# Kernel optimization log

Measured on AMD Instinct MI355X. Metric: run time of the kernel, lower is better.

Reference implementation:

```python
import jax, jax.numpy as jnp
import numpy as np

B, T, N, K, d = 8, 12, 325, 8, 64
D = K * d


def setup_inputs() -> dict:
    key = jax.random.key(0)
    ks = jax.random.split(key, 12)
    s = 0.02
    f32 = jnp.float32
    inp = {
        "X": jax.random.normal(ks[0], (B, T, N, D), f32),
        "STE": jax.random.normal(ks[1], (B, T, N, D), f32),
        "Wq": (jax.random.normal(ks[2], (2 * D, D), f32) * s),
        "bq": jnp.zeros((D,), f32),
        "Wk": (jax.random.normal(ks[3], (2 * D, D), f32) * s),
        "bk": jnp.zeros((D,), f32),
        "Wv": (jax.random.normal(ks[4], (2 * D, D), f32) * s),
        "bv": jnp.zeros((D,), f32),
        "W1": (jax.random.normal(ks[5], (D, D), f32) * s),
        "b1": jnp.zeros((D,), f32),
        "W2": (jax.random.normal(ks[6], (D, D), f32) * s),
        "b2": jnp.zeros((D,), f32),
        "attn_mask": 0,
    }
    return inp


def reference(X, STE, Wq, bq, Wk, bk, Wv, bv, W1, b1, W2, b2, attn_mask):
    # X, STE: [B, T, N, D]
    Xc = jnp.concatenate([X, STE], axis=-1)          # [B,T,N,2D]
    q = jax.nn.relu(Xc @ Wq + bq).reshape(B, T, N, K, d)
    k = jax.nn.relu(Xc @ Wk + bk).reshape(B, T, N, K, d)
    v = jax.nn.relu(Xc @ Wv + bv).reshape(B, T, N, K, d)

    # scores: [B, K, T, N, N] (attention over spatial/node axis N)
    scores = jnp.einsum('btnhe,btmhe->bhtnm', q, k)
    # mask_flag=False -> TriangularCausalMask applied (upper-tri masked with -inf)
    causal = jnp.triu(jnp.ones((N, N), dtype=bool), 1)
    scores = jnp.where(causal, -jnp.inf, scores)
    # original scales AFTER masking; -inf / sqrt(d) stays -inf
    scores = scores / jnp.sqrt(jnp.asarray(d, scores.dtype))
    attn = jax.nn.softmax(scores, axis=-1)
    # dropout: eval mode (identity)

    ctx = jnp.einsum('bhtnm,btmhe->btnhe', attn, v).reshape(B, T, N, D)
    out = jax.nn.relu(ctx @ W1 + b1) @ W2 + b2        # [B,T,N,D]

    # match torch's head-major cat(dim=0): [K*B, T, N, N]
    attn_full = jnp.transpose(attn, (1, 0, 2, 3, 4)).reshape(K * B, T, N, N)
    return out, attn_full
```

## Files before the change

### kernel.cpp

```cpp
#include <hip/hip_runtime.h>
#include <hip/hip_bf16.h>

typedef __hip_bfloat16 bf16;
using f32x4  = __attribute__((ext_vector_type(4))) float;
using short8 = __attribute__((ext_vector_type(8))) short;

#define M_ROWS   31200
#define M_PAD    31232
#define N_TOK    325
#define D_MODEL  512
#define QKV_LD   1536

#define GLOBAL_AS(p) ((const __attribute__((address_space(1))) unsigned int*)(p))
#define LDS_AS(p)    ((__attribute__((address_space(3))) unsigned int*)(p))

__global__ void init_flag(int* flag) { if (threadIdx.x == 0) *flag = 0; }

__global__ void detect_dtype(const unsigned short* __restrict__ x, int* flag)
{
    int i = blockIdx.x * 256 + threadIdx.x;
    unsigned short h = x[i];
    int e = (h >> 7) & 0xFF;
    if (e >= 135) atomicOr(flag, 1);
}

__device__ __forceinline__ float load_in(const void* p, size_t i, bool f32)
{
    return f32 ? ((const float*)p)[i] : __bfloat162float(((const bf16*)p)[i]);
}

__global__ void concat_cast(const void* __restrict__ X, const void* __restrict__ STE,
                            bf16* __restrict__ Xc, const int* __restrict__ flag)
{
    const bool f32 = (*flag != 0);
    int idx = blockIdx.x * 256 + threadIdx.x;
    int r = idx >> 7, c8 = (idx & 127) << 3;
    short8 v = {0, 0, 0, 0, 0, 0, 0, 0};
    if (r < M_ROWS) {
        const void* src = (c8 < 512) ? X : STE;
        int cc = c8 & 511;
        if (f32) {
            const float* s = (const float*)src + (size_t)r * 512 + cc;
            float4 a = *(const float4*)s;
            float4 b = *(const float4*)(s + 4);
            ((bf16*)&v)[0] = __float2bfloat16(a.x); ((bf16*)&v)[1] = __float2bfloat16(a.y);
            ((bf16*)&v)[2] = __float2bfloat16(a.z); ((bf16*)&v)[3] = __float2bfloat16(a.w);
            ((bf16*)&v)[4] = __float2bfloat16(b.x); ((bf16*)&v)[5] = __float2bfloat16(b.y);
            ((bf16*)&v)[6] = __float2bfloat16(b.z); ((bf16*)&v)[7] = __float2bfloat16(b.w);
        } else {
            v = *(const short8*)((const bf16*)src + (size_t)r * 512 + cc);
        }
    }
    *(short8*)&Xc[(size_t)r * 1024 + c8] = v;
}

__global__ void transpose_w_tiled(const void* __restrict__ src, bf16* __restrict__ dst,
                                  int krows, int ncols, const int* __restrict__ flag)
{
    __shared__ float tile[32][33];
    const bool f32 = (*flag != 0);
    const int kt = blockIdx.y * 32, nt = blockIdx.x * 32;
    const int tx = threadIdx.x & 31, ty = threadIdx.x >> 5;
#pragma unroll
    for (int r = 0; r < 32; r += 8)
        tile[ty + r][tx] = load_in(src, (size_t)(kt + ty + r) * ncols + (nt + tx), f32);
    __syncthreads();
#pragma unroll
    for (int r = 0; r < 32; r += 8)
        dst[(size_t)(nt + ty + r) * krows + (kt + tx)] = __float2bfloat16(tile[tx][ty + r]);
}

__global__ void prep_bias(const void* __restrict__ bq, const void* __restrict__ bk,
                          const void* __restrict__ bv, const void* __restrict__ b1,
                          const void* __restrict__ b2,
                          float* __restrict__ biasQKV, float* __restrict__ b1f,
                          float* __restrict__ b2f, const int* __restrict__ flag)
{
    const bool f32 = (*flag != 0);
    int i = blockIdx.x * 256 + threadIdx.x;
    if (i < 512) {
        biasQKV[i]        = load_in(bq, i, f32);
        biasQKV[512 + i]  = load_in(bk, i, f32);
        biasQKV[1024 + i] = load_in(bv, i, f32);
        b1f[i] = load_in(b1, i, f32);
        b2f[i] = load_in(b2, i, f32);
    }
}

template<int OUTF32>
__global__ __launch_bounds__(256) void gemm_lds(
    const bf16* __restrict__ A, int lda,
    const bf16* __restrict__ Bt, int ldb,
    const float* __restrict__ bias, void* __restrict__ Cv,
    int Mvalid, int Kdim, int ldc, int do_relu, int nby)
{
    __shared__ alignas(16) bf16 As0[128 * 32];
    __shared__ alignas(16) bf16 As1[128 * 32];
    __shared__ alignas(16) bf16 Bs0[128 * 32];
    __shared__ alignas(16) bf16 Bs1[128 * 32];
    const int cpx = gridDim.x >> 3;
    const int swz = (blockIdx.x & 7) * cpx + (blockIdx.x >> 3);
    const int m0 = (swz / nby) * 128;
    const int n0 = (swz % nby) * 128;
    const int t = threadIdx.x, wave = t >> 6, lane = t & 63;
    const int wm = (wave >> 1) * 64, wn = (wave & 1) * 64;
    const int lrow = lane & 15, lk8 = (lane >> 4) * 8;
    const int srow = lane >> 2, scol = (lane & 3) << 3;
    f32x4 acc[4][4] = {};
    const int nk = Kdim >> 6;

    for (int ks = 0; ks < nk; ++ks) {
        const int kk = ks << 6;
        __syncthreads();
#pragma unroll
        for (int c = 0; c < 2; ++c) {
            const int chunk = wave * 2 + c;
            const bf16* ga = A  + (size_t)(m0 + chunk * 16 + srow) * lda + kk + scol;
            const bf16* gb = Bt + (size_t)(n0 + chunk * 16 + srow) * ldb + kk + scol;
            __builtin_amdgcn_global_load_lds(GLOBAL_AS(ga),      LDS_AS(As0 + chunk * 512), 16, 0, 0);
            __builtin_amdgcn_global_load_lds(GLOBAL_AS(ga + 32), LDS_AS(As1 + chunk * 512), 16, 0, 0);
            __builtin_amdgcn_global_load_lds(GLOBAL_AS(gb),      LDS_AS(Bs0 + chunk * 512), 16, 0, 0);
            __builtin_amdgcn_global_load_lds(GLOBAL_AS(gb + 32), LDS_AS(Bs1 + chunk * 512), 16, 0, 0);
        }
        __syncthreads();
        short8 af[4], bfr[4];
#pragma unroll
        for (int i = 0; i < 4; ++i) {
            af[i]  = *(const short8*)&As0[(wm + i * 16 + lrow) * 32 + lk8];
            bfr[i] = *(const short8*)&Bs0[(wn + i * 16 + lrow) * 32 + lk8];
        }
#pragma unroll
        for (int i = 0; i < 4; ++i)
#pragma unroll
            for (int j = 0; j < 4; ++j)
                acc[i][j] = __builtin_amdgcn_mfma_f32_16x16x32_bf16(
                    af[i], bfr[j], acc[i][j], 0, 0, 0);
#pragma unroll
        for (int i = 0; i < 4; ++i) {
            af[i]  = *(const short8*)&As1[(wm + i * 16 + lrow) * 32 + lk8];
            bfr[i] = *(const short8*)&Bs1[(wn + i * 16 + lrow) * 32 + lk8];
        }
#pragma unroll
        for (int i = 0; i < 4; ++i)
#pragma unroll
            for (int j = 0; j < 4; ++j)
                acc[i][j] = __builtin_amdgcn_mfma_f32_16x16x32_bf16(
                    af[i], bfr[j], acc[i][j], 0, 0, 0);
    }

    const int r4 = (lane >> 4) * 4;
#pragma unroll
    for (int i = 0; i < 4; ++i) {
#pragma unroll
        for (int r = 0; r < 4; ++r) {
            int grow = m0 + wm + i * 16 + r4 + r;
            if (OUTF32 && grow >= Mvalid) continue;
#pragma unroll
            for (int j = 0; j < 4; ++j) {
                int gcol = n0 + wn + j * 16 + lrow;
                float v  = acc[i][j][r] + bias[gcol];
                if (do_relu) v = fmaxf(v, 0.0f);
                if (OUTF32)
                    ((float*)Cv)[(size_t)grow * ldc + gcol] = v;
                else
                    ((bf16*)Cv)[(size_t)grow * ldc + gcol] = __float2bfloat16(v);
            }
        }
    }
}

__global__ __launch_bounds__(512) void gemm_lds256(
    const bf16* __restrict__ A, int lda,
    const bf16* __restrict__ Bt, int ldb,
    const float* __restrict__ bias, bf16* __restrict__ C,
    int Kdim, int ldc, int nby)
{
    __shared__ alignas(16) bf16 As0[256 * 32];
    __shared__ alignas(16) bf16 As1[256 * 32];
    __shared__ alignas(16) bf16 Bs0[128 * 32];
    __shared__ alignas(16) bf16 Bs1[128 * 32];
    const int cpx = gridDim.x >> 3;
    const int swz = (blockIdx.x & 7) * cpx + (blockIdx.x >> 3);
    const int m0 = (swz / nby) * 256;
    const int n0 = (swz % nby) * 128;
    const int t = threadIdx.x, wave = t >> 6, lane = t & 63;
    const int wm = (wave >> 1) * 64, wn = (wave & 1) * 64;
    const int lrow = lane & 15, lk8 = (lane >> 4) * 8;
    const int srow = lane >> 2, scol = (lane & 3) << 3;
    f32x4 acc[4][4] = {};
    const int nk = Kdim >> 6;

    for (int ks = 0; ks < nk; ++ks) {
        const int kk = ks << 6;
        __syncthreads();
#pragma unroll
        for (int c = 0; c < 2; ++c) {
            const int arow = wave * 32 + c * 16;
            const bf16* ga = A + (size_t)(m0 + arow + srow) * lda + kk + scol;
            __builtin_amdgcn_global_load_lds(GLOBAL_AS(ga),      LDS_AS(As0 + arow * 32), 16, 0, 0);
            __builtin_amdgcn_global_load_lds(GLOBAL_AS(ga + 32), LDS_AS(As1 + arow * 32), 16, 0, 0);
        }
        {
            const int brow = wave * 16;
            const bf16* gb = Bt + (size_t)(n0 + brow + srow) * ldb + kk + scol;
            __builtin_amdgcn_global_load_lds(GLOBAL_AS(gb),      LDS_AS(Bs0 + brow * 32), 16, 0, 0);
            __builtin_amdgcn_global_load_lds(GLOBAL_AS(gb + 32), LDS_AS(Bs1 + brow * 32), 16, 0, 0);
        }
        __syncthreads();
        short8 af[4], bfr[4];
#pragma unroll
        for (int i = 0; i < 4; ++i) {
            af[i]  = *(const short8*)&As0[(wm + i * 16 + lrow) * 32 + lk8];
            bfr[i] = *(const short8*)&Bs0[(wn + i * 16 + lrow) * 32 + lk8];
        }
#pragma unroll
        for (int i = 0; i < 4; ++i)
#pragma unroll
            for (int j = 0; j < 4; ++j)
                acc[i][j] = __builtin_amdgcn_mfma_f32_16x16x32_bf16(
                    af[i], bfr[j], acc[i][j], 0, 0, 0);
#pragma unroll
        for (int i = 0; i < 4; ++i) {
            af[i]  = *(const short8*)&As1[(wm + i * 16 + lrow) * 32 + lk8];
            bfr[i] = *(const short8*)&Bs1[(wn + i * 16 + lrow) * 32 + lk8];
        }
#pragma unroll
        for (int i = 0; i < 4; ++i)
#pragma unroll
            for (int j = 0; j < 4; ++j)
                acc[i][j] = __builtin_amdgcn_mfma_f32_16x16x32_bf16(
                    af[i], bfr[j], acc[i][j], 0, 0, 0);
    }

    const int r4 = (lane >> 4) * 4;
#pragma unroll
    for (int i = 0; i < 4; ++i) {
#pragma unroll
        for (int r = 0; r < 4; ++r) {
            int grow = m0 + wm + i * 16 + r4 + r;
#pragma unroll
            for (int j = 0; j < 4; ++j) {
                int gcol = n0 + wn + j * 16 + lrow;
                float v  = fmaxf(acc[i][j][r] + bias[gcol], 0.0f);
                C[(size_t)grow * ldc + gcol] = __float2bfloat16(v);
            }
        }
    }
}

#define KS_LD  72
#define VT_LD  354
__global__ __launch_bounds__(512) void attn_kernel(
    bf16* __restrict__ qkv, float* __restrict__ attn_out)
{
    __shared__ alignas(16) bf16 Ks[336 * KS_LD];
    __shared__ alignas(16) bf16 Vt[64 * VT_LD + 32];
    __shared__ alignas(16) bf16 ptile[8][16 * 40];
    const int t = threadIdx.x, lane = t & 63, w = t >> 6;
    const int h = blockIdx.x & 7, bt = blockIdx.x >> 3;
    const size_t rowbase = (size_t)bt * N_TOK;
    const int lrow = lane & 15, lk8 = (lane >> 4) * 8;
    const int r4 = (lane >> 4) * 4;
    const int b = bt / 12, tt2 = bt % 12;
    const size_t hb_base = (((size_t)(h * 8 + b)) * 12 + tt2) * N_TOK;

    for (int task = t; task < 336 * 8; task += 512) {
        int m = task >> 3, e0 = (task & 7) << 3;
        short8 v = {0, 0, 0, 0, 0, 0, 0, 0};
        if (m < N_TOK)
            v = *(const short8*)(qkv + (rowbase + m) * QKV_LD + 512 + h * 64 + e0);
        *(short8*)&Ks[m * KS_LD + e0] = v;
    }
    for (int task = t; task < 352 * 8; task += 512) {
        int m = task >> 3, e0 = (task & 7) << 3;
        short8 v = {0, 0, 0, 0, 0, 0, 0, 0};
        if (m < N_TOK)
            v = *(const short8*)(qkv + (rowbase + m) * QKV_LD + 1024 + h * 64 + e0);
#pragma unroll
        for (int j = 0; j < 8; ++j)
            Vt[(e0 + j) * VT_LD + m] = ((bf16*)&v)[j];
    }
    __syncthreads();

    for (int it = 0; it < 3; ++it) {
        if (it == 2 && w > 4) break;
        const int tile = (it < 2) ? (w + it * 8) : (20 - w);
        const int r0 = tile * 16;

        int qrow = r0 + lrow; if (qrow > N_TOK - 1) qrow = N_TOK - 1;
        const bf16* qp = qkv + (rowbase + qrow) * QKV_LD + h * 64 + lk8;
        short8 qa0 = *(const short8*)(qp);
        short8 qa1 = *(const short8*)(qp + 32);

        f32x4 f[22];
        f[21] = (f32x4){0.f, 0.f, 0.f, 0.f};
#pragma unroll
        for (int ct = 0; ct < 21; ++ct) {
            if (ct <= tile) {
                f32x4 a = {0.f, 0.f, 0.f, 0.f};
                short8 kb0 = *(const short8*)&Ks[(ct * 16 + lrow) * KS_LD + lk8];
                short8 kb1 = *(const short8*)&Ks[(ct * 16 + lrow) * KS_LD + 32 + lk8];
                a = __builtin_amdgcn_mfma_f32_16x16x32_bf16(qa0, kb0, a, 0, 0, 0);
                a = __builtin_amdgcn_mfma_f32_16x16x32_bf16(qa1, kb1, a, 0, 0, 0);
                f[ct] = a;
            }
        }

        float mx[4] = {-1e30f, -1e30f, -1e30f, -1e30f};
        float sm[4] = {0.f, 0.f, 0.f, 0.f};
#pragma unroll
        for (int ct = 0; ct < 21; ++ct) {
            if (ct <= tile) {
                const int c = ct * 16 + lrow;
#pragma unroll
                for (int r = 0; r < 4; ++r)
                    if (c <= r0 + r4 + r) mx[r] = fmaxf(mx[r], f[ct][r]);
            }
        }
#pragma unroll
        for (int r = 0; r < 4; ++r) {
#pragma unroll
            for (int o = 1; o < 16; o <<= 1) mx[r] = fmaxf(mx[r], __shfl_xor(mx[r], o));
        }
#pragma unroll
        for (int ct = 0; ct < 21; ++ct) {
            if (ct <= tile) {
                const int c = ct * 16 + lrow;
#pragma unroll
                for (int r = 0; r < 4; ++r) {
                    float e = (c <= r0 + r4 + r)
                                  ? __expf((f[ct][r] - mx[r]) * 0.125f) : 0.f;
                    f[ct][r] = e;
                    sm[r] += e;
                }
            }
        }
#pragma unroll
        for (int r = 0; r < 4; ++r) {
#pragma unroll
            for (int o = 1; o < 16; o <<= 1) sm[r] += __shfl_xor(sm[r], o);
            sm[r] = 1.0f / sm[r];
        }
#pragma unroll
        for (int ct = 0; ct < 21; ++ct) {
            if (ct <= tile) {
#pragma unroll
                for (int r = 0; r < 4; ++r) f[ct][r] *= sm[r];
            }
        }

#pragma unroll
        for (int ct = 0; ct < 21; ++ct) {
            const int c = ct * 16 + lrow;
            if (c < N_TOK) {
#pragma unroll
                for (int r = 0; r < 4; ++r) {
                    const int n = r0 + r4 + r;
                    if (n < N_TOK) {
                        float v = (ct <= tile && c <= n) ? f[ct][r] : 0.f;
                        attn_out[(hb_base + n) * N_TOK + c] = v;
                    }
                }
            }
        }

        f32x4 acc[4] = {};
        bf16* pt = &ptile[w][0];
#pragma unroll
        for (int s = 0; s < 11; ++s) {
            if (s <= (tile >> 1)) {
#pragma unroll
                for (int half = 0; half < 2; ++half) {
                    const int ct2 = 2 * s + half;
                    const int c = ct2 * 16 + lrow;
#pragma unroll
                    for (int r = 0; r < 4; ++r) {
                        const int n = r0 + r4 + r;
                        float v = (ct2 <= tile && c <= n) ? f[ct2][r] : 0.f;
                        pt[(r4 + r) * 40 + half * 16 + lrow] = __float2bfloat16(v);
                    }
                }
                short8 aa = *(const short8*)&pt[lrow * 40 + lk8];
#pragma unroll
                for (int e = 0; e < 4; ++e) {
                    short8 bb = *(const short8*)&Vt[(e * 16 + lrow) * VT_LD + s * 32 + lk8];
                    acc[e] = __builtin_amdgcn_mfma_f32_16x16x32_bf16(aa, bb, acc[e], 0, 0, 0);
                }
            }
        }

#pragma unroll
        for (int e = 0; e < 4; ++e) {
#pragma unroll
            for (int r = 0; r < 4; ++r) {
                const int n = r0 + r4 + r;
                if (n < N_TOK)
                    qkv[(rowbase + n) * QKV_LD + h * 64 + e * 16 + lrow] =
                        __float2bfloat16(acc[e][r]);
            }
        }
    }
}

extern "C" void kernel_launch(void* const* d_in, const int* in_sizes, int n_in,
                              void* d_out, int out_size, void* d_ws, size_t ws_size,
                              hipStream_t stream)
{
    const void* X   = d_in[0];
    const void* STE = d_in[1];
    const void* Wq  = d_in[2];
    const void* bq  = d_in[3];
    const void* Wk  = d_in[4];
    const void* bk  = d_in[5];
    const void* Wv  = d_in[6];
    const void* bv  = d_in[7];
    const void* W1  = d_in[8];
    const void* b1  = d_in[9];
    const void* W2  = d_in[10];
    const void* b2  = d_in[11];

    float* out0     = (float*)d_out;
    float* attn_out = (float*)d_out + (size_t)M_ROWS * D_MODEL;
    bf16*  Xc       = (bf16*)attn_out;

    char* ws = (char*)d_ws;
    bf16*  qkv   = (bf16*)(ws);
    bf16*  BtQKV = (bf16*)(ws + 95944704);
    bf16*  W1T   = (bf16*)(ws + 99090432);
    bf16*  W2T   = (bf16*)(ws + 99614720);
    float* biasQ = (float*)(ws + 100139008);
    float* b1f   = (float*)(ws + 100145152);
    float* b2f   = (float*)(ws + 100147200);
    int*   flag  = (int*)(ws + 100149248);
    bf16*  hbuf  = qkv + 512;

    init_flag<<<1, 64, 0, stream>>>(flag);
    detect_dtype<<<64, 256, 0, stream>>>((const unsigned short*)X, flag);

    transpose_w_tiled<<<dim3(16, 32), 256, 0, stream>>>(Wq, BtQKV, 1024, 512, flag);
    transpose_w_tiled<<<dim3(16, 32), 256, 0, stream>>>(Wk, BtQKV + 512 * 1024, 1024, 512, flag);
    transpose_w_tiled<<<dim3(16, 32), 256, 0, stream>>>(Wv, BtQKV + 1024 * 1024, 1024, 512, flag);
    transpose_w_tiled<<<dim3(16, 16), 256, 0, stream>>>(W1, W1T, 512, 512, flag);
    transpose_w_tiled<<<dim3(16, 16), 256, 0, stream>>>(W2, W2T, 512, 512, flag);
    prep_bias<<<2, 256, 0, stream>>>(bq, bk, bv, b1, b2, biasQ, b1f, b2f, flag);

    concat_cast<<<(M_PAD * 128) / 256, 256, 0, stream>>>(X, STE, Xc, flag);

    gemm_lds256<<<122 * 12, 512, 0, stream>>>(
        Xc, 1024, BtQKV, 1024, biasQ, qkv, 1024, QKV_LD, 12);

    attn_kernel<<<768, 512, 0, stream>>>(qkv, attn_out);

    gemm_lds<0><<<244 * 4, 256, 0, stream>>>(
        qkv, QKV_LD, W1T, 512, b1f, hbuf, M_PAD, 512, QKV_LD, 1, 4);

    gemm_lds<1><<<244 * 4, 256, 0, stream>>>(
        hbuf, QKV_LD, W2T, 512, b2f, out0, M_ROWS, 512, D_MODEL, 0, 4);
}
```

Measured before the change: 403.4 us.

## Fuse concat/cast into QKV GEMM and use 256-row tiles for FFN GEMMs

Removes the separate concat_cast kernel. The QKV GEMM now reads X and STE directly, converts fp32 to bf16 in registers and stores the A tiles to LDS, which avoids writing and re-reading a 64MB bf16 intermediate. The two FFN GEMMs move from the 128x128 kernel to the templated 256x128 kernel with 512 threads, halving the block count. The trade-off is that the A loads are now synchronous register loads instead of async global_load_lds, which may expose latency inside the GEMM main loop.

```diff
diff --git a/kernel.cpp b/kernel.cpp
--- a/kernel.cpp
+++ b/kernel.cpp
@@ -27,31 +27,6 @@
 __device__ __forceinline__ float load_in(const void* p, size_t i, bool f32)
 {
     return f32 ? ((const float*)p)[i] : __bfloat162float(((const bf16*)p)[i]);
-}
-
-__global__ void concat_cast(const void* __restrict__ X, const void* __restrict__ STE,
-                            bf16* __restrict__ Xc, const int* __restrict__ flag)
-{
-    const bool f32 = (*flag != 0);
-    int idx = blockIdx.x * 256 + threadIdx.x;
-    int r = idx >> 7, c8 = (idx & 127) << 3;
-    short8 v = {0, 0, 0, 0, 0, 0, 0, 0};
-    if (r < M_ROWS) {
-        const void* src = (c8 < 512) ? X : STE;
-        int cc = c8 & 511;
-        if (f32) {
-            const float* s = (const float*)src + (size_t)r * 512 + cc;
-            float4 a = *(const float4*)s;
-            float4 b = *(const float4*)(s + 4);
-            ((bf16*)&v)[0] = __float2bfloat16(a.x); ((bf16*)&v)[1] = __float2bfloat16(a.y);
-            ((bf16*)&v)[2] = __float2bfloat16(a.z); ((bf16*)&v)[3] = __float2bfloat16(a.w);
-            ((bf16*)&v)[4] = __float2bfloat16(b.x); ((bf16*)&v)[5] = __float2bfloat16(b.y);
-            ((bf16*)&v)[6] = __float2bfloat16(b.z); ((bf16*)&v)[7] = __float2bfloat16(b.w);
-        } else {
-            v = *(const short8*)((const bf16*)src + (size_t)r * 512 + cc);
-        }
-    }
-    *(short8*)&Xc[(size_t)r * 1024 + c8] = v;
 }
 
 __global__ void transpose_w_tiled(const void* __restrict__ src, bf16* __restrict__ dst,
@@ -87,40 +62,65 @@
     }
 }
 
-template<int OUTF32>
-__global__ __launch_bounds__(256) void gemm_lds(
-    const bf16* __restrict__ A, int lda,
-    const bf16* __restrict__ Bt, int ldb,
-    const float* __restrict__ bias, void* __restrict__ Cv,
-    int Mvalid, int Kdim, int ldc, int do_relu, int nby)
-{
-    __shared__ alignas(16) bf16 As0[128 * 32];
-    __shared__ alignas(16) bf16 As1[128 * 32];
+__global__ __launch_bounds__(512) void gemm_qkv(
+    const void* __restrict__ Xv, const void* __restrict__ STEv,
+    const bf16* __restrict__ Bt, const float* __restrict__ bias,
+    bf16* __restrict__ C, const int* __restrict__ flag)
+{
+    __shared__ alignas(16) bf16 As0[256 * 32];
+    __shared__ alignas(16) bf16 As1[256 * 32];
     __shared__ alignas(16) bf16 Bs0[128 * 32];
     __shared__ alignas(16) bf16 Bs1[128 * 32];
+    const bool f32 = (*flag != 0);
     const int cpx = gridDim.x >> 3;
     const int swz = (blockIdx.x & 7) * cpx + (blockIdx.x >> 3);
-    const int m0 = (swz / nby) * 128;
-    const int n0 = (swz % nby) * 128;
+    const int m0 = (swz / 12) * 256;
+    const int n0 = (swz % 12) * 128;
     const int t = threadIdx.x, wave = t >> 6, lane = t & 63;
     const int wm = (wave >> 1) * 64, wn = (wave & 1) * 64;
     const int lrow = lane & 15, lk8 = (lane >> 4) * 8;
     const int srow = lane >> 2, scol = (lane & 3) << 3;
     f32x4 acc[4][4] = {};
-    const int nk = Kdim >> 6;
-
-    for (int ks = 0; ks < nk; ++ks) {
+
+    for (int ks = 0; ks < 16; ++ks) {
         const int kk = ks << 6;
+        const void* src = (kk < 512) ? Xv : STEv;
+        const int kc = kk & 511;
         __syncthreads();
 #pragma unroll
         for (int c = 0; c < 2; ++c) {
-            const int chunk = wave * 2 + c;
-            const bf16* ga = A  + (size_t)(m0 + chunk * 16 + srow) * lda + kk + scol;
-            const bf16* gb = Bt + (size_t)(n0 + chunk * 16 + srow) * ldb + kk + scol;
-            __builtin_amdgcn_global_load_lds(GLOBAL_AS(ga),      LDS_AS(As0 + chunk * 512), 16, 0, 0);
-            __builtin_amdgcn_global_load_lds(GLOBAL_AS(ga + 32), LDS_AS(As1 + chunk * 512), 16, 0, 0);
-            __builtin_amdgcn_global_load_lds(GLOBAL_AS(gb),      LDS_AS(Bs0 + chunk * 512), 16, 0, 0);
-            __builtin_amdgcn_global_load_lds(GLOBAL_AS(gb + 32), LDS_AS(Bs1 + chunk * 512), 16, 0, 0);
+            const int arow = wave * 32 + c * 16;
+            const int grow = m0 + arow + srow;
+            short8 va0 = {0,0,0,0,0,0,0,0}, va1 = {0,0,0,0,0,0,0,0};
+            if (grow < M_ROWS) {
+                if (f32) {
+                    const float* s = (const float*)src + (size_t)grow * 512 + kc + scol;
+                    float4 a0 = *(const float4*)(s);
+                    float4 a1 = *(const float4*)(s + 4);
+                    float4 b0 = *(const float4*)(s + 32);
+                    float4 b1 = *(const float4*)(s + 36);
+                    ((bf16*)&va0)[0] = __float2bfloat16(a0.x); ((bf16*)&va0)[1] = __float2bfloat16(a0.y);
+                    ((bf16*)&va0)[2] = __float2bfloat16(a0.z); ((bf16*)&va0)[3] = __float2bfloat16(a0.w);
+                    ((bf16*)&va0)[4] = __float2bfloat16(a1.x); ((bf16*)&va0)[5] = __float2bfloat16(a1.y);
+                    ((bf16*)&va0)[6] = __float2bfloat16(a1.z); ((bf16*)&va0)[7] = __float2bfloat16(a1.w);
+                    ((bf16*)&va1)[0] = __float2bfloat16(b0.x); ((bf16*)&va1)[1] = __float2bfloat16(b0.y);
+                    ((bf16*)&va1)[2] = __float2bfloat16(b0.z); ((bf16*)&va1)[3] = __float2bfloat16(b0.w);
+                    ((bf16*)&va1)[4] = __float2bfloat16(b1.x); ((bf16*)&va1)[5] = __float2bfloat16(b1.y);
+                    ((bf16*)&va1)[6] = __float2bfloat16(b1.z); ((bf16*)&va1)[7] = __float2bfloat16(b1.w);
+                } else {
+                    const bf16* s = (const bf16*)src + (size_t)grow * 512 + kc + scol;
+                    va0 = *(const short8*)(s);
+                    va1 = *(const short8*)(s + 32);
+                }
+            }
+            *(short8*)&As0[(arow + srow) * 32 + scol] = va0;
+            *(short8*)&As1[(arow + srow) * 32 + scol] = va1;
+        }
+        {
+            const int brow = wave * 16;
+            const bf16* gb = Bt + (size_t)(n0 + brow + srow) * 1024 + kk + scol;
+            __builtin_amdgcn_global_load_lds(GLOBAL_AS(gb),      LDS_AS(Bs0 + brow * 32), 16, 0, 0);
+            __builtin_amdgcn_global_load_lds(GLOBAL_AS(gb + 32), LDS_AS(Bs1 + brow * 32), 16, 0, 0);
         }
         __syncthreads();
         short8 af[4], bfr[4];
@@ -154,26 +154,22 @@
 #pragma unroll
         for (int r = 0; r < 4; ++r) {
             int grow = m0 + wm + i * 16 + r4 + r;
-            if (OUTF32 && grow >= Mvalid) continue;
 #pragma unroll
             for (int j = 0; j < 4; ++j) {
                 int gcol = n0 + wn + j * 16 + lrow;
-                float v  = acc[i][j][r] + bias[gcol];
-                if (do_relu) v = fmaxf(v, 0.0f);
-                if (OUTF32)
-                    ((float*)Cv)[(size_t)grow * ldc + gcol] = v;
-                else
-                    ((bf16*)Cv)[(size_t)grow * ldc + gcol] = __float2bfloat16(v);
-            }
-        }
-    }
-}
-
+                float v  = fmaxf(acc[i][j][r] + bias[gcol], 0.0f);
+                C[(size_t)grow * QKV_LD + gcol] = __float2bfloat16(v);
+            }
+        }
+    }
+}
+
+template<int OUTF32, int RELU>
 __global__ __launch_bounds__(512) void gemm_lds256(
     const bf16* __restrict__ A, int lda,
     const bf16* __restrict__ Bt, int ldb,
-    const float* __restrict__ bias, bf16* __restrict__ C,
-    int Kdim, int ldc, int nby)
+    const float* __restrict__ bias, void* __restrict__ Cv,
+    int Mvalid, int Kdim, int ldc, int nby)
 {
     __shared__ alignas(16) bf16 As0[256 * 32];
     __shared__ alignas(16) bf16 As1[256 * 32];
@@ -238,11 +234,16 @@
 #pragma unroll
         for (int r = 0; r < 4; ++r) {
             int grow = m0 + wm + i * 16 + r4 + r;
+            if (OUTF32 && grow >= Mvalid) continue;
 #pragma unroll
             for (int j = 0; j < 4; ++j) {
                 int gcol = n0 + wn + j * 16 + lrow;
-                float v  = fmaxf(acc[i][j][r] + bias[gcol], 0.0f);
-                C[(size_t)grow * ldc + gcol] = __float2bfloat16(v);
+                float v  = acc[i][j][r] + bias[gcol];
+                if (RELU) v = fmaxf(v, 0.0f);
+                if (OUTF32)
+                    ((float*)Cv)[(size_t)grow * ldc + gcol] = v;
+                else
+                    ((bf16*)Cv)[(size_t)grow * ldc + gcol] = __float2bfloat16(v);
             }
         }
     }
@@ -421,7 +422,6 @@
 
     float* out0     = (float*)d_out;
     float* attn_out = (float*)d_out + (size_t)M_ROWS * D_MODEL;
-    bf16*  Xc       = (bf16*)attn_out;
 
     char* ws = (char*)d_ws;
     bf16*  qkv   = (bf16*)(ws);
@@ -444,16 +444,13 @@
     transpose_w_tiled<<<dim3(16, 16), 256, 0, stream>>>(W2, W2T, 512, 512, flag);
     prep_bias<<<2, 256, 0, stream>>>(bq, bk, bv, b1, b2, biasQ, b1f, b2f, flag);
 
-    concat_cast<<<(M_PAD * 128) / 256, 256, 0, stream>>>(X, STE, Xc, flag);
-
-    gemm_lds256<<<122 * 12, 512, 0, stream>>>(
-        Xc, 1024, BtQKV, 1024, biasQ, qkv, 1024, QKV_LD, 12);
+    gemm_qkv<<<122 * 12, 512, 0, stream>>>(X, STE, BtQKV, biasQ, qkv, flag);
 
     attn_kernel<<<768, 512, 0, stream>>>(qkv, attn_out);
 
-    gemm_lds<0><<<244 * 4, 256, 0, stream>>>(
-        qkv, QKV_LD, W1T, 512, b1f, hbuf, M_PAD, 512, QKV_LD, 1, 4);
-
-    gemm_lds<1><<<244 * 4, 256, 0, stream>>>(
-        hbuf, QKV_LD, W2T, 512, b2f, out0, M_ROWS, 512, D_MODEL, 0, 4);
-}
+    gemm_lds256<0, 1><<<122 * 4, 512, 0, stream>>>(
+        qkv, QKV_LD, W1T, 512, b1f, hbuf, M_PAD, 512, QKV_LD, 4);
+
+    gemm_lds256<1, 0><<<122 * 4, 512, 0, stream>>>(
+        hbuf, QKV_LD, W2T, 512, b2f, out0, M_ROWS, 512, D_MODEL, 4);
+}
```

Measured after the change: 412.9 us. +2.3%, slower.
